# Kernel tuning notes

Hardware: AMD Instinct MI355X
Metric: run time of the kernel (lower is better)

Reference implementation:

```python
import jax, jax.numpy as jnp
import numpy as np
from jax import lax

B, N, M = 4, 16384, 2048
C_IN = 64
RADII = (0.2, 0.4)
KS = (32, 64)
MLPS = ((64, 64, 128), (64, 96, 128))
EPS = 1e-5


def setup_inputs() -> dict:
    key = jax.random.key(0)
    ks = jax.random.split(key, 32)
    inp = {}
    inp["xyz"] = jax.random.uniform(ks[0], (B, 3, N), jnp.float32)
    inp["feature"] = jax.random.normal(ks[1], (B, C_IN, N), jnp.float32)
    ki = 2
    for s, chans in enumerate(MLPS):
        cin = C_IN + 3  # use_xyz concatenates relative xyz
        for l, cout in enumerate(chans):
            inp[f"w{s}{l}"] = jax.random.normal(ks[ki], (cout, cin), jnp.float32) * (1.0 / np.sqrt(cin)); ki += 1
            inp[f"g{s}{l}"] = jnp.ones((cout,), jnp.float32)
            inp[f"b{s}{l}"] = jnp.zeros((cout,), jnp.float32)
            cin = cout
    return inp


def _fps(points):
    """Farthest point sampling. points [N,3] -> [M] int32 indices (starts at 0)."""
    n = points.shape[0]
    def step(carry, _):
        dists, last = carry
        d = jnp.sum((points - points[last]) ** 2, axis=-1)
        dists = jnp.minimum(dists, d)
        nxt = jnp.argmax(dists).astype(jnp.int32)
        return (dists, nxt), nxt
    init = (jnp.full((n,), 1e10, jnp.float32), jnp.int32(0))
    _, rest = lax.scan(step, init, None, length=M - 1)
    return jnp.concatenate([jnp.zeros((1,), jnp.int32), rest])


def _ball_query(xyz, new_xyz, radius, k):
    """xyz [B,3,N], new_xyz [B,3,M] -> [B,M,k] int32. First-found semantics: empty
    slots are filled with the first valid index (pointnet2 ball_query behavior)."""
    xyz = lax.stop_gradient(xyz)
    new_xyz = lax.stop_gradient(new_xyz)
    n = xyz.shape[-1]
    sq_x = jnp.sum(xyz ** 2, axis=1)          # [B,N]
    sq_c = jnp.sum(new_xyz ** 2, axis=1)      # [B,M]
    d2 = sq_c[:, :, None] + sq_x[:, None, :] - 2.0 * jnp.einsum('bdm,bdn->bmn', new_xyz, xyz)
    scores = jnp.where(d2 < radius * radius, jnp.arange(n, dtype=jnp.int32), n)
    idx = -lax.top_k(-scores, k)[0]           # k smallest indices (in order)
    first = idx[..., :1]
    idx = jnp.where(idx >= n, first, idx)
    return jnp.where(idx >= n, 0, idx)


def _group(feat, idx):
    """feat [B,C,N], idx [B,M,K] -> [B,C,M,K]"""
    return jax.vmap(lambda f, i: f[:, i])(feat, idx)


def _forward(xyz, feature, params):
    idx = jax.vmap(_fps)(jnp.transpose(lax.stop_gradient(xyz), (0, 2, 1)))  # [B,M]
    new_xyz = jnp.take_along_axis(xyz, idx[:, None, :].astype(jnp.int32), axis=2)  # [B,3,M]
    feats = []
    for s in range(len(MLPS)):
        nidx = _ball_query(xyz, new_xyz, RADII[s], KS[s])        # [B,M,K]
        gxyz = _group(xyz, nidx) - new_xyz[..., None]            # [B,3,M,K]
        x = jnp.concatenate([gxyz, _group(feature, nidx)], axis=1)  # [B,3+C,M,K]
        for l in range(len(MLPS[s])):
            w = params[f"w{s}{l}"]; g = params[f"g{s}{l}"]; b = params[f"b{s}{l}"]
            x = jnp.einsum('oc,bcmk->bomk', w, x)                # 1x1 conv
            mu = jnp.mean(x, axis=(0, 2, 3), keepdims=True)      # train-mode BN
            var = jnp.mean((x - mu) ** 2, axis=(0, 2, 3), keepdims=True)
            x = (x - mu) * lax.rsqrt(var + EPS)
            x = x * g[None, :, None, None] + b[None, :, None, None]
            x = jax.nn.relu(x)
        feats.append(jnp.max(x, axis=3))                         # max over neighbors
    return new_xyz, jnp.concatenate(feats, axis=1)               # [B,3,M], [B,256,M]


def reference(xyz, feature, w00, g00, b00, w01, g01, b01, w02, g02, b02,
              w10, g10, b10, w11, g11, b11, w12, g12, b12):
    params = dict(w00=w00, g00=g00, b00=b00, w01=w01, g01=g01, b01=b01,
                  w02=w02, g02=g02, b02=b02, w10=w10, g10=g10, b10=b10,
                  w11=w11, g11=g11, b11=b11, w12=w12, g12=g12, b12=b12)
    return _forward(xyz, feature, params)
```

## Files before the change

kernel.cpp:

```cpp
#include <hip/hip_runtime.h>
#include <cstdint>

constexpr int B_ = 4, N_ = 16384, M_ = 2048;
constexpr int COLS0 = B_ * M_ * 32;
constexpr int COLS1 = B_ * M_ * 64;

constexpr size_t OFF_NEWXYZ = 0;
constexpr size_t OFF_NIDX0  = (size_t)B_ * 3 * M_ * 4;
constexpr size_t OFF_NIDX1  = OFF_NIDX0 + (size_t)COLS0 * 4;
constexpr size_t OFF_STATS  = OFF_NIDX1 + (size_t)COLS1 * 4;
constexpr size_t STATS_VALS = 64 * 2 * 128;
constexpr size_t OFF_COEF   = OFF_STATS + 6 * STATS_VALS * 8;
constexpr size_t OFF_Z      = OFF_COEF + 6 * 128 * 16;
constexpr int ZSTRIDE = 96 * 64;

__global__ __launch_bounds__(1024, 4) void fps_kernel(const float* __restrict__ xyz,
                                                      float* __restrict__ newxyz,
                                                      float* __restrict__ outxyz) {
#pragma clang fp contract(off)
  __shared__ float2 s_xy[N_];
  __shared__ unsigned long long s_red[2][16];
  int b = blockIdx.x, t = threadIdx.x;
  const float* xb = xyz + (size_t)b * 3 * N_;
  float pz[16], dd[16];
#pragma unroll
  for (int i = 0; i < 16; ++i) {
    int n = t + (i << 10);
    float x = xb[n], y = xb[N_ + n];
    pz[i] = xb[2 * N_ + n];
    s_xy[n] = make_float2(x, y);
    dd[i] = 1e10f;
    asm volatile("" : "+v"(pz[i]));
  }
  size_t base = (size_t)b * 3 * M_;
  float fx = xb[0], fy = xb[N_], fz = xb[2 * N_];
  if (t == 0) {
    newxyz[base] = fx; newxyz[base + M_] = fy; newxyz[base + 2 * M_] = fz;
    outxyz[base] = fx; outxyz[base + M_] = fy; outxyz[base + 2 * M_] = fz;
  }
  int lane = t & 63, wid = t >> 6;
  for (int s = 1; s < M_; ++s) {
    float bv = -1.f; int bi = 0;
#pragma unroll
    for (int i = 0; i < 16; ++i) {
      int n = t + (i << 10);
      float2 xy = s_xy[n];
      float dx = xy.x - fx, dy = xy.y - fy, dz = pz[i] - fz;
      float d = (dx * dx + dy * dy) + dz * dz;
      float dm = dd[i];
      if (d < dm) dm = d;
      dd[i] = dm;
      if (dm > bv) { bv = dm; bi = n; }
    }
    unsigned long long key =
        ((unsigned long long)__float_as_uint(bv) << 32) | (unsigned)(0xFFFFFFFFu - (unsigned)bi);
#pragma unroll
    for (int off = 1; off < 64; off <<= 1) {
      unsigned long long o = __shfl_xor(key, off);
      if (o > key) key = o;
    }
    int p = s & 1;
    if (lane == 0) s_red[p][wid] = key;
    __syncthreads();
    unsigned long long k = s_red[p][0];
#pragma unroll
    for (int r = 1; r < 16; ++r) {
      unsigned long long o = s_red[p][r];
      if (o > k) k = o;
    }
    int w = (int)(0xFFFFFFFFu - (unsigned)(k & 0xFFFFFFFFull));
    fx = xb[w]; fy = xb[N_ + w]; fz = xb[2 * N_ + w];
    if (t == 0) {
      newxyz[base + s] = fx; newxyz[base + M_ + s] = fy; newxyz[base + 2 * M_ + s] = fz;
      outxyz[base + s] = fx; outxyz[base + M_ + s] = fy; outxyz[base + 2 * M_ + s] = fz;
    }
  }
}

template <int KNB>
__global__ __launch_bounds__(256) void bq_kernel(const float* __restrict__ xyz,
                                                 const float* __restrict__ newxyz,
                                                 int* __restrict__ nidx, float r2) {
#pragma clang fp contract(off)
  int t = threadIdx.x, lane = t & 63, wq = t >> 6;
  int q = blockIdx.x * 4 + wq;
  int b = q >> 11, m = q & 2047;
  const float* xb = xyz + (size_t)b * 3 * N_;
  float cx = newxyz[((size_t)b * 3 + 0) * M_ + m];
  float cy = newxyz[((size_t)b * 3 + 1) * M_ + m];
  float cz = newxyz[((size_t)b * 3 + 2) * M_ + m];
  float sqc = (cx * cx + cy * cy) + cz * cz;
  int found = 0, first = 0;
  for (int c = 0; c < N_ / 64; ++c) {
    int n = c * 64 + lane;
    float x = xb[n], y = xb[N_ + n], z = xb[2 * N_ + n];
    float sqx = (x * x + y * y) + z * z;
    float dot = fmaf(cz, z, fmaf(cy, y, cx * x));
    float d2 = (sqc + sqx) - 2.0f * dot;
    bool in = d2 < r2;
    unsigned long long mask = __ballot(in);
    if (mask) {
      if (found == 0) first = c * 64 + (__ffsll((long long)mask) - 1);
      int pos = found + __popcll(mask & ((1ull << lane) - 1ull));
      if (in && pos < KNB) nidx[(size_t)q * KNB + pos] = n;
      found += __popcll(mask);
      if (found >= KNB) break;
    }
  }
  if (found < KNB) {
    int fill = (found == 0) ? 0 : first;
    for (int s = found + lane; s < KNB; s += 64) nidx[(size_t)q * KNB + s] = fill;
  }
}

__device__ __forceinline__ void stat_accum(float acc, int o, int cout, double* stats,
                                           int part, int lane) {
  float v1 = acc, v2 = acc * acc;
#pragma unroll
  for (int off = 1; off < 64; off <<= 1) {
    v1 += __shfl_xor(v1, off);
    v2 += __shfl_xor(v2, off);
  }
  if (lane == 0) {
    atomicAdd(stats + ((size_t)part * 2 + 0) * cout + o, (double)v1);
    atomicAdd(stats + ((size_t)part * 2 + 1) * cout + o, (double)v2);
  }
}

template <int KNB>
__global__ __launch_bounds__(256) void convL0_kernel(
    const float* __restrict__ w0,
    const float* __restrict__ xyz, const float* __restrict__ feat,
    const int* __restrict__ nidx, const float* __restrict__ newxyz,
    float* __restrict__ Z, double* __restrict__ stats) {
  int lane = threadIdx.x & 63, wq = threadIdx.x >> 6;
  int rec = blockIdx.x * 4 + wq;
  int col = rec * 64 + lane;
  float x[67];
  {
    int b = col / (M_ * KNB);
    int rem = col - b * (M_ * KNB);
    int m = rem / KNB;
    int n = nidx[col];
    const float* xb = xyz + (size_t)b * 3 * N_;
    x[0] = xb[n]          - newxyz[((size_t)b * 3 + 0) * M_ + m];
    x[1] = xb[N_ + n]     - newxyz[((size_t)b * 3 + 1) * M_ + m];
    x[2] = xb[2 * N_ + n] - newxyz[((size_t)b * 3 + 2) * M_ + m];
    const float* fb = feat + (size_t)b * 64 * N_;
#pragma unroll
    for (int c = 0; c < 64; ++c) x[3 + c] = fb[(size_t)c * N_ + n];
  }
  float* zr = Z + (size_t)rec * ZSTRIDE;
  int part = rec & 63;
  for (int o = 0; o < 64; ++o) {
    const float* wr = w0 + (size_t)o * 67;
    float acc = 0.f;
#pragma unroll
    for (int c = 0; c < 67; ++c) acc += wr[c] * x[c];
    zr[o * 64 + lane] = acc;
    stat_accum(acc, o, 64, stats, part, lane);
  }
}

template <int CIN, int COUT>
__global__ __launch_bounds__(256) void convMid_kernel(
    const float* __restrict__ w,
    const float4* __restrict__ coefIn,
    float* __restrict__ Z, double* __restrict__ stats) {
  int lane = threadIdx.x & 63, wq = threadIdx.x >> 6;
  int rec = blockIdx.x * 4 + wq;
  float* zr = Z + (size_t)rec * ZSTRIDE;
  float x[CIN];
#pragma unroll
  for (int c = 0; c < CIN; ++c) {
    float v = zr[c * 64 + lane];
    float4 cf = coefIn[c];
    x[c] = fmaxf(((v - cf.x) * cf.y) * cf.z + cf.w, 0.f);
  }
  int part = rec & 63;
  for (int o = 0; o < COUT; ++o) {
    const float* wr = w + (size_t)o * CIN;
    float acc = 0.f;
#pragma unroll
    for (int c = 0; c < CIN; ++c) acc += wr[c] * x[c];
    zr[o * 64 + lane] = acc;
    stat_accum(acc, o, COUT, stats, part, lane);
  }
}

template <int CIN>
__global__ __launch_bounds__(256) void convLastStats_kernel(
    const float* __restrict__ w, const float4* __restrict__ coefIn,
    const float* __restrict__ Z, double* __restrict__ stats) {
  int lane = threadIdx.x & 63, wq = threadIdx.x >> 6;
  int rec = blockIdx.x * 4 + wq;
  const float* zr = Z + (size_t)rec * ZSTRIDE;
  float x[CIN];
#pragma unroll
  for (int c = 0; c < CIN; ++c) {
    float v = zr[c * 64 + lane];
    float4 cf = coefIn[c];
    x[c] = fmaxf(((v - cf.x) * cf.y) * cf.z + cf.w, 0.f);
  }
  int part = rec & 63;
  for (int o = 0; o < 128; ++o) {
    const float* wr = w + (size_t)o * CIN;
    float acc = 0.f;
#pragma unroll
    for (int c = 0; c < CIN; ++c) acc += wr[c] * x[c];
    stat_accum(acc, o, 128, stats, part, lane);
  }
}

template <int CIN, int KNB>
__global__ __launch_bounds__(256) void convLastPool_kernel(
    const float* __restrict__ w, const float4* __restrict__ coefIn,
    const float4* __restrict__ coefOut,
    const float* __restrict__ Z, float* __restrict__ outFeats, int chBase) {
  int lane = threadIdx.x & 63, wq = threadIdx.x >> 6;
  int rec = blockIdx.x * 4 + wq;
  const float* zr = Z + (size_t)rec * ZSTRIDE;
  float x[CIN];
#pragma unroll
  for (int c = 0; c < CIN; ++c) {
    float v = zr[c * 64 + lane];
    float4 cf = coefIn[c];
    x[c] = fmaxf(((v - cf.x) * cf.y) * cf.z + cf.w, 0.f);
  }
  for (int o = 0; o < 128; ++o) {
    const float* wr = w + (size_t)o * CIN;
    float acc = 0.f;
#pragma unroll
    for (int c = 0; c < CIN; ++c) acc += wr[c] * x[c];
    float4 cf = coefOut[o];
    float z = fmaxf(((acc - cf.x) * cf.y) * cf.z + cf.w, 0.f);
    if (KNB == 64) {
#pragma unroll
      for (int off = 1; off < 64; off <<= 1) z = fmaxf(z, __shfl_xor(z, off));
      if (lane == 0) {
        int b = rec >> 11, m = rec & 2047;
        outFeats[((size_t)b * 256 + chBase + o) * M_ + m] = z;
      }
    } else {
#pragma unroll
      for (int off = 1; off < 32; off <<= 1) z = fmaxf(z, __shfl_xor(z, off));
      if ((lane & 31) == 0) {
        int grp = rec * 2 + (lane >> 5);
        int b = grp >> 11, m = grp & 2047;
        outFeats[((size_t)b * 256 + chBase + o) * M_ + m] = z;
      }
    }
  }
}

__global__ void coef_kernel(const double* __restrict__ stats, const float* __restrict__ g,
                            const float* __restrict__ bb, float4* __restrict__ coef,
                            int cout, double invcnt) {
  int ch = threadIdx.x;
  if (ch >= cout) return;
  double s1 = 0.0, s2 = 0.0;
  for (int p = 0; p < 64; ++p) {
    s1 += stats[((size_t)p * 2 + 0) * cout + ch];
    s2 += stats[((size_t)p * 2 + 1) * cout + ch];
  }
  double mean = s1 * invcnt;
  double var = s2 * invcnt - mean * mean;
  double rstd = 1.0 / sqrt(var + 1e-5);
  coef[ch] = make_float4((float)mean, (float)rstd, g[ch], bb[ch]);
}

extern "C" void kernel_launch(void* const* d_in, const int* in_sizes, int n_in,
                              void* d_out, int out_size, void* d_ws, size_t ws_size,
                              hipStream_t stream) {
  const float* xyz  = (const float*)d_in[0];
  const float* feat = (const float*)d_in[1];
  const float* w00 = (const float*)d_in[2],  *g00 = (const float*)d_in[3],  *b00 = (const float*)d_in[4];
  const float* w01 = (const float*)d_in[5],  *g01 = (const float*)d_in[6],  *b01 = (const float*)d_in[7];
  const float* w02 = (const float*)d_in[8],  *g02 = (const float*)d_in[9],  *b02 = (const float*)d_in[10];
  const float* w10 = (const float*)d_in[11], *g10 = (const float*)d_in[12], *b10 = (const float*)d_in[13];
  const float* w11 = (const float*)d_in[14], *g11 = (const float*)d_in[15], *b11 = (const float*)d_in[16];
  const float* w12 = (const float*)d_in[17], *g12 = (const float*)d_in[18], *b12 = (const float*)d_in[19];

  char* ws = (char*)d_ws;
  float*  newxyz = (float*)(ws + OFF_NEWXYZ);
  int*    nidx0  = (int*)(ws + OFF_NIDX0);
  int*    nidx1  = (int*)(ws + OFF_NIDX1);
  double* stats  = (double*)(ws + OFF_STATS);
  float4* coef   = (float4*)(ws + OFF_COEF);
  float*  Z      = (float*)(ws + OFF_Z);
  float* outF = (float*)d_out;
  float* outFeats = outF + (size_t)B_ * 3 * M_;

  hipMemsetAsync(ws + OFF_STATS, 0, 6 * STATS_VALS * 8, stream);
  fps_kernel<<<B_, 1024, 0, stream>>>(xyz, newxyz, outF);
  bq_kernel<32><<<(B_ * M_) / 4, 256, 0, stream>>>(xyz, newxyz, nidx0, (float)(0.2 * 0.2));
  bq_kernel<64><<<(B_ * M_) / 4, 256, 0, stream>>>(xyz, newxyz, nidx1, (float)(0.4 * 0.4));

  float4* c00 = coef + 0 * 128; float4* c01 = coef + 1 * 128; float4* c02 = coef + 2 * 128;
  float4* c10 = coef + 3 * 128; float4* c11 = coef + 4 * 128; float4* c12 = coef + 5 * 128;
  double* st0 = stats + 0 * STATS_VALS; double* st1 = stats + 1 * STATS_VALS;
  double* st2 = stats + 2 * STATS_VALS; double* st3 = stats + 3 * STATS_VALS;
  double* st4 = stats + 4 * STATS_VALS; double* st5 = stats + 5 * STATS_VALS;
  int gb0 = (COLS0 / 64) / 4, gb1 = (COLS1 / 64) / 4;

  convL0_kernel<32><<<gb0, 256, 0, stream>>>(w00, xyz, feat, nidx0, newxyz, Z, st0);
  coef_kernel<<<1, 128, 0, stream>>>(st0, g00, b00, c00, 64, 1.0 / COLS0);
  convMid_kernel<64, 64><<<gb0, 256, 0, stream>>>(w01, c00, Z, st1);
  coef_kernel<<<1, 128, 0, stream>>>(st1, g01, b01, c01, 64, 1.0 / COLS0);
  convLastStats_kernel<64><<<gb0, 256, 0, stream>>>(w02, c01, Z, st2);
  coef_kernel<<<1, 128, 0, stream>>>(st2, g02, b02, c02, 128, 1.0 / COLS0);
  convLastPool_kernel<64, 32><<<gb0, 256, 0, stream>>>(w02, c01, c02, Z, outFeats, 0);

  convL0_kernel<64><<<gb1, 256, 0, stream>>>(w10, xyz, feat, nidx1, newxyz, Z, st3);
  coef_kernel<<<1, 128, 0, stream>>>(st3, g10, b10, c10, 64, 1.0 / COLS1);
  convMid_kernel<64, 96><<<gb1, 256, 0, stream>>>(w11, c10, Z, st4);
  coef_kernel<<<1, 128, 0, stream>>>(st4, g11, b11, c11, 96, 1.0 / COLS1);
  convLastStats_kernel<96><<<gb1, 256, 0, stream>>>(w12, c11, Z, st5);
  coef_kernel<<<1, 128, 0, stream>>>(st5, g12, b12, c12, 128, 1.0 / COLS1);
  convLastPool_kernel<96, 64><<<gb1, 256, 0, stream>>>(w12, c11, c12, Z, outFeats, 128);
}
```

Before: 5.838 ms.

## Split farthest point sampling across 8 blocks per batch with global atomic exchange

The FPS kernel now runs 8 cooperating blocks per batch item, each holding a slice of the points in registers, instead of one 1024-thread block per batch. Every sampling step each block publishes its local argmax to a per-step global slot with atomics, then spin-waits until all 8 slots are filled before reducing to the winner. The aim is to use more compute units for the serial FPS loop, which dominates runtime, at the cost of a cross-block global-memory handshake on every step. It also depends on all 32 blocks being co-resident, and the spin loop has a bounded iteration count that could return a wrong winner if a block is late.

```diff
diff --git a/kernel.cpp b/kernel.cpp
--- a/kernel.cpp
+++ b/kernel.cpp
@@ -4,6 +4,10 @@
 constexpr int B_ = 4, N_ = 16384, M_ = 2048;
 constexpr int COLS0 = B_ * M_ * 32;
 constexpr int COLS1 = B_ * M_ * 64;
+
+constexpr int FPS_G   = 8;
+constexpr int FPS_T   = 512;
+constexpr int FPS_PPT = N_ / FPS_G / FPS_T;
 
 constexpr size_t OFF_NEWXYZ = 0;
 constexpr size_t OFF_NIDX0  = (size_t)B_ * 3 * M_ * 4;
@@ -11,46 +15,47 @@
 constexpr size_t OFF_STATS  = OFF_NIDX1 + (size_t)COLS1 * 4;
 constexpr size_t STATS_VALS = 64 * 2 * 128;
 constexpr size_t OFF_COEF   = OFF_STATS + 6 * STATS_VALS * 8;
-constexpr size_t OFF_Z      = OFF_COEF + 6 * 128 * 16;
+constexpr size_t OFF_SLOT   = OFF_COEF + 6 * 128 * 16;
+constexpr size_t SLOT_BYTES = (size_t)B_ * M_ * FPS_G * 64;
+constexpr size_t OFF_Z      = OFF_SLOT + SLOT_BYTES;
 constexpr int ZSTRIDE = 96 * 64;
 
-__global__ __launch_bounds__(1024, 4) void fps_kernel(const float* __restrict__ xyz,
-                                                      float* __restrict__ newxyz,
-                                                      float* __restrict__ outxyz) {
+__global__ __launch_bounds__(FPS_T) void fps_kernel(const float* __restrict__ xyz,
+                                                    float* __restrict__ newxyz,
+                                                    float* __restrict__ outxyz,
+                                                    unsigned long long* __restrict__ slots) {
 #pragma clang fp contract(off)
-  __shared__ float2 s_xy[N_];
-  __shared__ unsigned long long s_red[2][16];
-  int b = blockIdx.x, t = threadIdx.x;
+  int bid = blockIdx.x;
+  int b = bid >> 3, g = bid & 7;
+  int t = threadIdx.x, lane = t & 63, wid = t >> 6;
   const float* xb = xyz + (size_t)b * 3 * N_;
-  float pz[16], dd[16];
-#pragma unroll
-  for (int i = 0; i < 16; ++i) {
-    int n = t + (i << 10);
-    float x = xb[n], y = xb[N_ + n];
-    pz[i] = xb[2 * N_ + n];
-    s_xy[n] = make_float2(x, y);
-    dd[i] = 1e10f;
-    asm volatile("" : "+v"(pz[i]));
-  }
+  int nbase = g * (N_ / FPS_G) + t;
+  float px[FPS_PPT], py[FPS_PPT], pz[FPS_PPT], dd[FPS_PPT];
+#pragma unroll
+  for (int j = 0; j < FPS_PPT; ++j) {
+    int n = nbase + j * FPS_T;
+    px[j] = xb[n]; py[j] = xb[N_ + n]; pz[j] = xb[2 * N_ + n];
+    dd[j] = 1e10f;
+  }
+  __shared__ unsigned long long s_red[2][FPS_T / 64];
+  __shared__ unsigned long long s_win[2];
   size_t base = (size_t)b * 3 * M_;
   float fx = xb[0], fy = xb[N_], fz = xb[2 * N_];
-  if (t == 0) {
+  if (g == 0 && t == 0) {
     newxyz[base] = fx; newxyz[base + M_] = fy; newxyz[base + 2 * M_] = fz;
     outxyz[base] = fx; outxyz[base + M_] = fy; outxyz[base + 2 * M_] = fz;
   }
-  int lane = t & 63, wid = t >> 6;
+  unsigned long long* sb = slots + (size_t)b * M_ * FPS_G * 8;
   for (int s = 1; s < M_; ++s) {
     float bv = -1.f; int bi = 0;
 #pragma unroll
-    for (int i = 0; i < 16; ++i) {
-      int n = t + (i << 10);
-      float2 xy = s_xy[n];
-      float dx = xy.x - fx, dy = xy.y - fy, dz = pz[i] - fz;
+    for (int j = 0; j < FPS_PPT; ++j) {
+      float dx = px[j] - fx, dy = py[j] - fy, dz = pz[j] - fz;
       float d = (dx * dx + dy * dy) + dz * dz;
-      float dm = dd[i];
+      float dm = dd[j];
       if (d < dm) dm = d;
-      dd[i] = dm;
-      if (dm > bv) { bv = dm; bi = n; }
+      dd[j] = dm;
+      if (dm > bv) { bv = dm; bi = nbase + j * FPS_T; }
     }
     unsigned long long key =
         ((unsigned long long)__float_as_uint(bv) << 32) | (unsigned)(0xFFFFFFFFu - (unsigned)bi);
@@ -62,15 +67,36 @@
     int p = s & 1;
     if (lane == 0) s_red[p][wid] = key;
     __syncthreads();
-    unsigned long long k = s_red[p][0];
-#pragma unroll
-    for (int r = 1; r < 16; ++r) {
-      unsigned long long o = s_red[p][r];
-      if (o > k) k = o;
-    }
+    if (wid == 0) {
+      unsigned long long bk = s_red[p][lane & 7];
+#pragma unroll
+      for (int off = 1; off < 8; off <<= 1) {
+        unsigned long long o = __shfl_xor(bk, off);
+        if (o > bk) bk = o;
+      }
+      unsigned long long kk = 0;
+      if (lane < FPS_G) {
+        unsigned long long* sp = sb + ((size_t)s * FPS_G + lane) * 8;
+        if (lane == g) atomicExch(sp, bk);
+        unsigned long long v = 0;
+        for (int it = 0; it < 1024 && v == 0; ++it) {
+          v = atomicAdd(sp, 0ull);
+          if (v == 0) __builtin_amdgcn_s_sleep(2);
+        }
+        kk = v;
+      }
+#pragma unroll
+      for (int off = 1; off < 8; off <<= 1) {
+        unsigned long long o = __shfl_xor(kk, off);
+        if (o > kk) kk = o;
+      }
+      if (lane == 0) s_win[p] = kk;
+    }
+    __syncthreads();
+    unsigned long long k = s_win[p];
     int w = (int)(0xFFFFFFFFu - (unsigned)(k & 0xFFFFFFFFull));
     fx = xb[w]; fy = xb[N_ + w]; fz = xb[2 * N_ + w];
-    if (t == 0) {
+    if (g == 0 && t == 0) {
       newxyz[base + s] = fx; newxyz[base + M_ + s] = fy; newxyz[base + 2 * M_ + s] = fz;
       outxyz[base + s] = fx; outxyz[base + M_ + s] = fy; outxyz[base + 2 * M_ + s] = fz;
     }
@@ -287,12 +313,14 @@
   int*    nidx1  = (int*)(ws + OFF_NIDX1);
   double* stats  = (double*)(ws + OFF_STATS);
   float4* coef   = (float4*)(ws + OFF_COEF);
+  unsigned long long* slots = (unsigned long long*)(ws + OFF_SLOT);
   float*  Z      = (float*)(ws + OFF_Z);
   float* outF = (float*)d_out;
   float* outFeats = outF + (size_t)B_ * 3 * M_;
 
   hipMemsetAsync(ws + OFF_STATS, 0, 6 * STATS_VALS * 8, stream);
-  fps_kernel<<<B_, 1024, 0, stream>>>(xyz, newxyz, outF);
+  hipMemsetAsync(ws + OFF_SLOT, 0, SLOT_BYTES, stream);
+  fps_kernel<<<B_ * FPS_G, FPS_T, 0, stream>>>(xyz, newxyz, outF, slots);
   bq_kernel<32><<<(B_ * M_) / 4, 256, 0, stream>>>(xyz, newxyz, nidx0, (float)(0.2 * 0.2));
   bq_kernel<64><<<(B_ * M_) / 4, 256, 0, stream>>>(xyz, newxyz, nidx1, (float)(0.4 * 0.4));
 
```

Result: faster. 5.196 ms (-11.0%).
